# Optimization experiments

Hardware: AMD Instinct MI355X
Metric: run time of the kernel (lower is better)

## Reference

```python
import jax, jax.numpy as jnp
import numpy as np

HIDDEN = 256

def setup_inputs() -> dict:
    key = jax.random.key(0)
    ks = jax.random.split(key, 8)
    B, T, D, O, H = 128, 1024, 512, 128, HIDDEN
    s_ih = 1.0 / np.sqrt(H)
    inp = {
        "input_x": jax.random.normal(ks[0], (B, T, D), dtype=jnp.float32),
        # PyTorch LSTM params, gate order (i, f, g, o)
        "W_ih": jax.random.uniform(ks[1], (4 * H, D), minval=-s_ih, maxval=s_ih, dtype=jnp.float32),
        "W_hh": jax.random.uniform(ks[2], (4 * H, H), minval=-s_ih, maxval=s_ih, dtype=jnp.float32),
        "b_ih": jax.random.uniform(ks[3], (4 * H,), minval=-s_ih, maxval=s_ih, dtype=jnp.float32),
        "b_hh": jax.random.uniform(ks[4], (4 * H,), minval=-s_ih, maxval=s_ih, dtype=jnp.float32),
        "W_out": jax.random.uniform(ks[5], (O, H), minval=-s_ih, maxval=s_ih, dtype=jnp.float32),
        "b_out": jax.random.uniform(ks[6], (O,), minval=-s_ih, maxval=s_ih, dtype=jnp.float32),
    }
    return inp

def _lstm_last_hidden(input_x, W_ih, W_hh, b_ih, b_hh):
    B, T, D = input_x.shape
    H = HIDDEN
    # Batch the input projection over all timesteps (one big GEMM): [B,T,4H]
    xg = jnp.einsum("btd,gd->btg", input_x, W_ih) + b_ih + b_hh
    xg = jnp.transpose(xg, (1, 0, 2))  # [T,B,4H] for scan over time

    def step(carry, xg_t):
        h, c = carry
        gates = xg_t + h @ W_hh.T  # [B,4H]
        i, f, g, o = jnp.split(gates, 4, axis=-1)
        i = jax.nn.sigmoid(i)
        f = jax.nn.sigmoid(f)
        g = jnp.tanh(g)
        o = jax.nn.sigmoid(o)
        c = f * c + i * g
        h = o * jnp.tanh(c)
        return (h, c), None

    h0 = jnp.zeros((B, H), dtype=input_x.dtype)
    c0 = jnp.zeros((B, H), dtype=input_x.dtype)
    (h_T, _), _ = jax.lax.scan(step, (h0, c0), xg)
    return h_T  # == y[:, -1, :]

def reference(input_x, W_ih, W_hh, b_ih, b_hh, W_out, b_out):
    h_T = _lstm_last_hidden(input_x, W_ih, W_hh, b_ih, b_hh)
    # Dropout is identity in eval mode; squeeze(dim=1) is a no-op for O>1.
    return h_T @ W_out.T + b_out  # [B, O]
```

## Files before the change

### kernel.cpp

```cpp
#include <hip/hip_runtime.h>
#include <hip/hip_bf16.h>

#define B_ 128
#define T_ 1024
#define D_ 512
#define H_ 256
#define G_ 1024

typedef __bf16 bf16_t;
typedef __bf16 bf16x8 __attribute__((ext_vector_type(8)));
typedef __bf16 bf16x4 __attribute__((ext_vector_type(4)));
typedef float  f32x4  __attribute__((ext_vector_type(4)));

__device__ __forceinline__ float fast_rcp(float x) { return __builtin_amdgcn_rcpf(x); }

__device__ __forceinline__ float sigmoid_f(float x) {
  return fast_rcp(1.0f + __expf(-x));
}
__device__ __forceinline__ float tanh_f(float x) {
  x = fminf(fmaxf(x, -15.0f), 15.0f);
  float e = __expf(-2.0f * x);
  return (1.0f - e) * fast_rcp(1.0f + e);
}

__device__ __forceinline__ void barrier_lds_only() {
  asm volatile("s_waitcnt lgkmcnt(0)\n\ts_barrier" ::: "memory");
}

__global__ __launch_bounds__(256) void prep_kernel(
    const float* __restrict__ Whh, const float* __restrict__ bih,
    const float* __restrict__ bhh, bf16_t* __restrict__ whhb,
    float* __restrict__ bias) {
  int i = blockIdx.x * 256 + threadIdx.x;
  if (i < G_ * H_) whhb[i] = (bf16_t)Whh[i];
  if (i < G_) bias[i] = bih[i] + bhh[i];
}

__global__ __launch_bounds__(512) void xg_gemm(
    const float* __restrict__ X, const float* __restrict__ Wih,
    const float* __restrict__ bias, bf16_t* __restrict__ xg2) {
  __shared__ __align__(16) bf16_t As[128][72];
  __shared__ __align__(16) bf16_t Bs[256][72];

  const int tid = threadIdx.x;
  const int lane = tid & 63;
  const int w = tid >> 6;
  const int q = lane >> 4;
  const int l15 = lane & 15;
  const int m0 = blockIdx.x * 128;
  const int ch0 = blockIdx.y * 64;

  f32x4 acc[16];
  #pragma unroll
  for (int n = 0; n < 16; ++n) acc[n] = (f32x4){0.f, 0.f, 0.f, 0.f};

  for (int kt = 0; kt < 8; ++kt) {
    const int k0 = kt * 64;
    __syncthreads();
    #pragma unroll
    for (int i = 0; i < 4; ++i) {
      int f = tid + 512 * i;
      int r = f >> 4, c4 = f & 15;
      float4 va = *(const float4*)(X + (size_t)(m0 + r) * D_ + k0 + c4 * 4);
      *(bf16x4*)&As[r][c4 * 4] =
          (bf16x4){(bf16_t)va.x, (bf16_t)va.y, (bf16_t)va.z, (bf16_t)va.w};
    }
    #pragma unroll
    for (int j = 0; j < 8; ++j) {
      int f = tid + 512 * j;
      int r = f >> 4, c4 = f & 15;
      int wr = (r >> 6) * 256 + ch0 + (r & 63);
      float4 vb = *(const float4*)(Wih + (size_t)wr * D_ + k0 + c4 * 4);
      *(bf16x4*)&Bs[r][c4 * 4] =
          (bf16x4){(bf16_t)vb.x, (bf16_t)vb.y, (bf16_t)vb.z, (bf16_t)vb.w};
    }
    __syncthreads();
    #pragma unroll
    for (int kk = 0; kk < 2; ++kk) {
      bf16x8 a = *(const bf16x8*)&As[16 * w + l15][kk * 32 + q * 8];
      #pragma unroll
      for (int n = 0; n < 16; ++n) {
        bf16x8 b = *(const bf16x8*)&Bs[16 * n + l15][kk * 32 + q * 8];
        acc[n] = __builtin_amdgcn_mfma_f32_16x16x32_bf16(a, b, acc[n], 0, 0, 0);
      }
    }
  }
  #pragma unroll
  for (int cs = 0; cs < 4; ++cs) {
    const int cc = ch0 + cs * 16 + l15;
    float bv0 = bias[cc], bv1 = bias[256 + cc];
    float bv2 = bias[512 + cc], bv3 = bias[768 + cc];
    #pragma unroll
    for (int i = 0; i < 4; ++i) {
      int row = m0 + 16 * w + 4 * q + i;
      bf16x4 v = (bf16x4){(bf16_t)(acc[cs][i] + bv0), (bf16_t)(acc[4 + cs][i] + bv1),
                          (bf16_t)(acc[8 + cs][i] + bv2), (bf16_t)(acc[12 + cs][i] + bv3)};
      *(bf16x4*)(xg2 + ((size_t)row * 256 + cc) * 4) = v;
    }
  }
}

__global__ __launch_bounds__(512, 2) void lstm_scan(
    const bf16_t* __restrict__ xg2, const bf16_t* __restrict__ Whh,
    float* __restrict__ hT) {
  __shared__ __align__(16) bf16_t wlds[8 * 16 * 512];
  __shared__ __align__(16) bf16_t hbuf[2][16][264];

  const int tid = threadIdx.x;
  const int lane = tid & 63;
  const int w = tid >> 6;
  const int q = lane >> 4;
  const int l15 = lane & 15;
  const int b0 = blockIdx.x * 8;
  const int rq = (q & 1) * 4 + (q >> 1) * 2;
  const bool hi = (lane >= 32);

  bf16x8 wreg[6][8];
  #pragma unroll
  for (int p2 = 0; p2 < 2; ++p2) {
    #pragma unroll
    for (int g2 = 0; g2 < 4; ++g2) {
      const int j = p2 * 4 + g2;
      const bf16_t* src =
          Whh + (size_t)(g2 * 256 + 32 * w + 16 * p2 + l15) * H_ + q * 8;
      #pragma unroll
      for (int kk = 0; kk < 8; ++kk) {
        bf16x8 v = *(const bf16x8*)(src + kk * 32);
        if (j < 6) {
          wreg[j][kk] = v;
        } else {
          *(bf16x8*)&wlds[(size_t)((w * 16 + (g2 - 2) * 8 + kk)) * 512 + lane * 8] = v;
        }
      }
    }
  }

  for (int i = tid; i < 2 * 16 * 264; i += 512) ((bf16_t*)hbuf)[i] = (bf16_t)0.0f;
  __syncthreads();

  float cst[2][2];
  #pragma unroll
  for (int p = 0; p < 2; ++p) { cst[p][0] = 0.f; cst[p][1] = 0.f; }

  const bf16_t* xp[2][2];
  #pragma unroll
  for (int p = 0; p < 2; ++p)
    #pragma unroll
    for (int k = 0; k < 2; ++k)
      xp[p][k] = xg2 + (size_t)(b0 + rq + k) * (size_t)T_ * 1024 + (32 * w + 16 * p + l15) * 4;

  bf16x4 xv[2][2], xn[2][2];
  #pragma unroll
  for (int p = 0; p < 2; ++p)
    #pragma unroll
    for (int k = 0; k < 2; ++k) {
      xv[p][k] = *(const bf16x4*)xp[p][k];
      xp[p][k] += 1024;
    }

  auto step = [&](int t, bf16x4 (&xc)[2][2], bf16x4 (&xf)[2][2]) {
    #pragma unroll
    for (int p = 0; p < 2; ++p)
      #pragma unroll
      for (int k = 0; k < 2; ++k) {
        xf[p][k] = *(const bf16x4*)xp[p][k];
        xp[p][k] += 1024;
      }
    const int cur = t & 1;
    #pragma unroll
    for (int p = 0; p < 2; ++p) {
      f32x4 acc[4];
      #pragma unroll
      for (int g = 0; g < 4; ++g) acc[g] = (f32x4){0.f, 0.f, 0.f, 0.f};
      #pragma unroll
      for (int kk = 0; kk < 8; ++kk) {
        bf16x8 a = *(const bf16x8*)&hbuf[cur][l15][kk * 32 + q * 8];
        if (p == 0) {
          acc[0] = __builtin_amdgcn_mfma_f32_16x16x32_bf16(a, wreg[0][kk], acc[0], 0, 0, 0);
          acc[1] = __builtin_amdgcn_mfma_f32_16x16x32_bf16(a, wreg[1][kk], acc[1], 0, 0, 0);
          acc[2] = __builtin_amdgcn_mfma_f32_16x16x32_bf16(a, wreg[2][kk], acc[2], 0, 0, 0);
          acc[3] = __builtin_amdgcn_mfma_f32_16x16x32_bf16(a, wreg[3][kk], acc[3], 0, 0, 0);
        } else {
          acc[0] = __builtin_amdgcn_mfma_f32_16x16x32_bf16(a, wreg[4][kk], acc[0], 0, 0, 0);
          acc[1] = __builtin_amdgcn_mfma_f32_16x16x32_bf16(a, wreg[5][kk], acc[1], 0, 0, 0);
          bf16x8 bg = *(const bf16x8*)&wlds[(size_t)(w * 16 + kk) * 512 + lane * 8];
          bf16x8 bo = *(const bf16x8*)&wlds[(size_t)(w * 16 + 8 + kk) * 512 + lane * 8];
          acc[2] = __builtin_amdgcn_mfma_f32_16x16x32_bf16(a, bg, acc[2], 0, 0, 0);
          acc[3] = __builtin_amdgcn_mfma_f32_16x16x32_bf16(a, bo, acc[3], 0, 0, 0);
        }
      }
      float G0[4], G1[4];
      #pragma unroll
      for (int g = 0; g < 4; ++g) {
        float s2 = __shfl(acc[g][2], lane ^ 32, 64);
        float s3 = __shfl(acc[g][3], lane ^ 32, 64);
        G0[g] = hi ? s2 : acc[g][0];
        G1[g] = hi ? s3 : acc[g][1];
      }
      const int c = 32 * w + 16 * p + l15;
      #pragma unroll
      for (int k = 0; k < 2; ++k) {
        const float* Gv_ = k ? G1 : G0;
        float gi = Gv_[0] + (float)xc[p][k][0];
        float gf = Gv_[1] + (float)xc[p][k][1];
        float gg = Gv_[2] + (float)xc[p][k][2];
        float go = Gv_[3] + (float)xc[p][k][3];
        float I = sigmoid_f(gi);
        float F = sigmoid_f(gf);
        float Gg = tanh_f(gg);
        float Ov = sigmoid_f(go);
        float cv = F * cst[p][k] + I * Gg;
        cst[p][k] = cv;
        float hv = Ov * tanh_f(cv);
        hbuf[cur ^ 1][rq + k][c] = (bf16_t)hv;
        if (t == T_ - 1) hT[(size_t)(b0 + rq + k) * H_ + c] = hv;
      }
    }
    barrier_lds_only();
  };

  #pragma unroll 1
  for (int t = 0; t < T_; t += 2) {
    step(t, xv, xn);
    step(t + 1, xn, xv);
  }
}

__global__ __launch_bounds__(128) void head_gemm(
    const float* __restrict__ hT, const float* __restrict__ Wout,
    const float* __restrict__ bout, float* __restrict__ out) {
  __shared__ float hrow[H_];
  const int b = blockIdx.x;
  const int o = threadIdx.x;
  hrow[o] = hT[(size_t)b * H_ + o];
  hrow[o + 128] = hT[(size_t)b * H_ + 128 + o];
  __syncthreads();
  float s = bout[o];
  const float* wr = Wout + (size_t)o * H_;
  #pragma unroll 8
  for (int j = 0; j < H_; ++j) s += hrow[j] * wr[j];
  out[(size_t)b * 128 + o] = s;
}

extern "C" void kernel_launch(void* const* d_in, const int* in_sizes, int n_in,
                              void* d_out, int out_size, void* d_ws, size_t ws_size,
                              hipStream_t stream) {
  const float* X    = (const float*)d_in[0];
  const float* Wih  = (const float*)d_in[1];
  const float* Whh  = (const float*)d_in[2];
  const float* bih  = (const float*)d_in[3];
  const float* bhh  = (const float*)d_in[4];
  const float* Wout = (const float*)d_in[5];
  const float* bout = (const float*)d_in[6];
  float* out = (float*)d_out;

  char* ws = (char*)d_ws;
  const size_t XG_BYTES   = (size_t)B_ * T_ * G_ * 2;
  const size_t WHHB_BYTES = (size_t)G_ * H_ * 2;
  const size_t BIAS_BYTES = (size_t)G_ * 4;
  bf16_t* xg2  = (bf16_t*)ws;
  bf16_t* whhb = (bf16_t*)(ws + XG_BYTES);
  float*  bias = (float*)(ws + XG_BYTES + WHHB_BYTES);
  float*  hT   = (float*)(ws + XG_BYTES + WHHB_BYTES + BIAS_BYTES);

  prep_kernel<<<dim3(1024), 256, 0, stream>>>(Whh, bih, bhh, whhb, bias);
  xg_gemm<<<dim3((B_ * T_) / 128, 4), 512, 0, stream>>>(X, Wih, bias, xg2);
  lstm_scan<<<dim3(B_ / 8), 512, 0, stream>>>(xg2, whhb, hT);
  head_gemm<<<dim3(B_), 128, 0, stream>>>(hT, Wout, bout, out);
}
```

Before: 3.337 ms.

## Pre-convert X and W_ih to bf16 and stream GEMM tiles via global_load_lds

Adds a path that first converts the input sequence and W_ih to bf16 in workspace. A new input-projection GEMM then loads tiles straight into LDS with global_load_lds, skipping the register-staged fp32-to-bf16 conversion inside the GEMM. This spends an extra full pass over X (read fp32, write bf16) and more workspace in exchange for a simpler, higher-throughput GEMM inner loop. The new path runs only when the workspace is large enough; otherwise the old path is used.

Result: faster. 3.179 ms (-4.8%).

```diff
diff --git a/kernel.cpp b/kernel.cpp
--- a/kernel.cpp
+++ b/kernel.cpp
@@ -25,6 +25,12 @@
 
 __device__ __forceinline__ void barrier_lds_only() {
   asm volatile("s_waitcnt lgkmcnt(0)\n\ts_barrier" ::: "memory");
+}
+
+__device__ __forceinline__ void gload_lds16(const void* g, void* l) {
+  __builtin_amdgcn_global_load_lds(
+      (const __attribute__((address_space(1))) void*)g,
+      (__attribute__((address_space(3))) void*)l, 16, 0, 0);
 }
 
 __global__ __launch_bounds__(256) void prep_kernel(
@@ -34,6 +40,92 @@
   int i = blockIdx.x * 256 + threadIdx.x;
   if (i < G_ * H_) whhb[i] = (bf16_t)Whh[i];
   if (i < G_) bias[i] = bih[i] + bhh[i];
+}
+
+__global__ __launch_bounds__(256) void prep_full_kernel(
+    const float* __restrict__ Whh, const float* __restrict__ bih,
+    const float* __restrict__ bhh, const float* __restrict__ Wih,
+    bf16_t* __restrict__ whhb, bf16_t* __restrict__ wihb,
+    float* __restrict__ bias) {
+  int i = blockIdx.x * 256 + threadIdx.x;
+  if (i < G_ * H_) whhb[i] = (bf16_t)Whh[i];
+  wihb[i] = (bf16_t)Wih[i];
+  if (i < G_) bias[i] = bih[i] + bhh[i];
+}
+
+__global__ __launch_bounds__(256) void xconv_kernel(
+    const float* __restrict__ X, bf16_t* __restrict__ Xb) {
+  const int n4 = (B_ * T_ * D_) / 4;
+  const int stride = gridDim.x * 256;
+  for (int i = blockIdx.x * 256 + threadIdx.x; i < n4; i += stride) {
+    float4 v = ((const float4*)X)[i];
+    ((bf16x4*)Xb)[i] =
+        (bf16x4){(bf16_t)v.x, (bf16_t)v.y, (bf16_t)v.z, (bf16_t)v.w};
+  }
+}
+
+__global__ __launch_bounds__(512) void xg_gemm_fast(
+    const bf16_t* __restrict__ Xb, const bf16_t* __restrict__ Wihb,
+    const float* __restrict__ bias, bf16_t* __restrict__ xg2) {
+  __shared__ __align__(16) bf16_t As[128][64];
+  __shared__ __align__(16) bf16_t Bs[256][64];
+
+  const int tid = threadIdx.x;
+  const int lane = tid & 63;
+  const int w = tid >> 6;
+  const int q = lane >> 4;
+  const int l15 = lane & 15;
+  const int m0 = blockIdx.x * 128;
+  const int ch0 = blockIdx.y * 64;
+
+  const int lr = lane >> 3;
+  const int lc = (lane & 7) * 8;
+
+  f32x4 acc[16];
+  #pragma unroll
+  for (int n = 0; n < 16; ++n) acc[n] = (f32x4){0.f, 0.f, 0.f, 0.f};
+
+  for (int kt = 0; kt < 8; ++kt) {
+    const int k0 = kt * 64;
+    __syncthreads();
+    #pragma unroll
+    for (int j = 0; j < 2; ++j) {
+      const int c = w * 2 + j;
+      gload_lds16(Xb + (size_t)(m0 + c * 8 + lr) * D_ + k0 + lc,
+                  (char*)&As[0][0] + c * 1024);
+    }
+    #pragma unroll
+    for (int j = 0; j < 4; ++j) {
+      const int c = w * 4 + j;
+      const int br = c * 8 + lr;
+      const int wr = (br >> 6) * 256 + ch0 + (br & 63);
+      gload_lds16(Wihb + (size_t)wr * D_ + k0 + lc,
+                  (char*)&Bs[0][0] + c * 1024);
+    }
+    __syncthreads();
+    #pragma unroll
+    for (int kk = 0; kk < 2; ++kk) {
+      bf16x8 a = *(const bf16x8*)&As[16 * w + l15][kk * 32 + q * 8];
+      #pragma unroll
+      for (int n = 0; n < 16; ++n) {
+        bf16x8 b = *(const bf16x8*)&Bs[16 * n + l15][kk * 32 + q * 8];
+        acc[n] = __builtin_amdgcn_mfma_f32_16x16x32_bf16(a, b, acc[n], 0, 0, 0);
+      }
+    }
+  }
+  #pragma unroll
+  for (int cs = 0; cs < 4; ++cs) {
+    const int cc = ch0 + cs * 16 + l15;
+    float bv0 = bias[cc], bv1 = bias[256 + cc];
+    float bv2 = bias[512 + cc], bv3 = bias[768 + cc];
+    #pragma unroll
+    for (int i = 0; i < 4; ++i) {
+      int row = m0 + 16 * w + 4 * q + i;
+      bf16x4 v = (bf16x4){(bf16_t)(acc[cs][i] + bv0), (bf16_t)(acc[4 + cs][i] + bv1),
+                          (bf16_t)(acc[8 + cs][i] + bv2), (bf16_t)(acc[12 + cs][i] + bv3)};
+      *(bf16x4*)(xg2 + ((size_t)row * 256 + cc) * 4) = v;
+    }
+  }
 }
 
 __global__ __launch_bounds__(512) void xg_gemm(
@@ -258,13 +350,27 @@
   const size_t XG_BYTES   = (size_t)B_ * T_ * G_ * 2;
   const size_t WHHB_BYTES = (size_t)G_ * H_ * 2;
   const size_t BIAS_BYTES = (size_t)G_ * 4;
+  const size_t HT_BYTES   = (size_t)B_ * H_ * 4;
+  const size_t WIHB_BYTES = (size_t)G_ * D_ * 2;
+  const size_t XB_BYTES   = (size_t)B_ * T_ * D_ * 2;
   bf16_t* xg2  = (bf16_t*)ws;
   bf16_t* whhb = (bf16_t*)(ws + XG_BYTES);
   float*  bias = (float*)(ws + XG_BYTES + WHHB_BYTES);
   float*  hT   = (float*)(ws + XG_BYTES + WHHB_BYTES + BIAS_BYTES);
-
-  prep_kernel<<<dim3(1024), 256, 0, stream>>>(Whh, bih, bhh, whhb, bias);
-  xg_gemm<<<dim3((B_ * T_) / 128, 4), 512, 0, stream>>>(X, Wih, bias, xg2);
+  bf16_t* wihb = (bf16_t*)(ws + XG_BYTES + WHHB_BYTES + BIAS_BYTES + HT_BYTES);
+  bf16_t* xb   = (bf16_t*)(ws + XG_BYTES + WHHB_BYTES + BIAS_BYTES + HT_BYTES + WIHB_BYTES);
+
+  const size_t NEED_FAST =
+      XG_BYTES + WHHB_BYTES + BIAS_BYTES + HT_BYTES + WIHB_BYTES + XB_BYTES;
+
+  if (ws_size >= NEED_FAST) {
+    prep_full_kernel<<<dim3(2048), 256, 0, stream>>>(Whh, bih, bhh, Wih, whhb, wihb, bias);
+    xconv_kernel<<<dim3(4096), 256, 0, stream>>>(X, xb);
+    xg_gemm_fast<<<dim3((B_ * T_) / 128, 4), 512, 0, stream>>>(xb, wihb, bias, xg2);
+  } else {
+    prep_kernel<<<dim3(1024), 256, 0, stream>>>(Whh, bih, bhh, whhb, bias);
+    xg_gemm<<<dim3((B_ * T_) / 128, 4), 512, 0, stream>>>(X, Wih, bias, xg2);
+  }
   lstm_scan<<<dim3(B_ / 8), 512, 0, stream>>>(xg2, whhb, hT);
   head_gemm<<<dim3(B_), 128, 0, stream>>>(hT, Wout, bout, out);
 }
```
